# Kernel optimization log

Hardware: AMD Instinct MI355X
Metric: run time of the kernel (lower is better)

Reference implementation:

```python
import jax, jax.numpy as jnp
import numpy as np

NUM_SRC = 100000
NUM_DST = 50000
E = 1200000
IN_FEATS = 128
H = 4
D = 16


def setup_inputs() -> dict:
    key = jax.random.key(0)
    ks = jax.random.split(key, 8)
    feat = jax.random.normal(ks[0], (NUM_DST + NUM_SRC, IN_FEATS), dtype=jnp.float32)
    edge_src = jax.random.randint(ks[1], (E,), 0, NUM_SRC)
    edge_dst = jax.random.randint(ks[2], (E,), 0, NUM_DST)
    # parameters (xavier-normal-ish scale)
    W = jax.random.normal(ks[3], (H * D, IN_FEATS), dtype=jnp.float32) * (2.0 / np.sqrt(IN_FEATS + H * D))
    attn_l = jax.random.normal(ks[4], (H, D), dtype=jnp.float32) * (2.0 / np.sqrt(1 + D))
    attn_r = jax.random.normal(ks[5], (H, D), dtype=jnp.float32) * (2.0 / np.sqrt(1 + D))
    bias = jnp.zeros((H * D,), dtype=jnp.float32)
    return {"feat": feat, "W": W, "attn_l": attn_l, "attn_r": attn_r,
            "bias": bias, "edge_src": edge_src, "edge_dst": edge_dst, "num_dst": NUM_DST}


def reference(feat, W, attn_l, attn_r, bias, edge_src, edge_dst, num_dst):
    negative_slope = 0.2
    n_heads, d_out = attn_l.shape
    # fc: [N, in] @ [in, H*D] -> [N, H, D]
    proj = (feat @ W.T).reshape(feat.shape[0], n_heads, d_out)
    feat_dst = proj[:num_dst]      # [num_dst, H, D]
    feat_src = proj[num_dst:]      # [num_src, H, D]
    el = jnp.einsum('nhd,hd->nh', feat_src, attn_l)  # [num_src, H]
    er = jnp.einsum('nhd,hd->nh', feat_dst, attn_r)  # [num_dst, H]
    # per-edge attention logits (u_add_v + leaky_relu)
    e = jax.nn.leaky_relu(el[edge_src] + er[edge_dst], negative_slope)  # [E, H]
    # segment softmax over destination neighborhoods
    m = jax.ops.segment_max(e, edge_dst, num_segments=num_dst)  # [num_dst, H]
    m = jnp.where(jnp.isfinite(m), m, 0.0)
    e_exp = jnp.exp(e - m[edge_dst])
    denom = jax.ops.segment_sum(e_exp, edge_dst, num_segments=num_dst)  # [num_dst, H]
    a = e_exp / denom[edge_dst]  # [E, H]
    # u_mul_e + sum scatter-aggregate
    msg = feat_src[edge_src] * a[:, :, None]  # [E, H, D]
    rst = jax.ops.segment_sum(msg, edge_dst, num_segments=num_dst)  # [num_dst, H, D]
    rst = rst + bias.reshape(1, n_heads, d_out)
    return rst
```

## Files before the change

kernel.cpp:

```cpp
#include <hip/hip_runtime.h>
#include <hip/hip_bf16.h>


#define NEG_SLOPE 0.2f
#define BSHIFT 7
#define BMASK  127
#define MAXBUK 512
#define FSH    12
#define FCAP   4096
#define EB     2048

typedef __attribute__((ext_vector_type(8))) short bf16x8;
typedef __attribute__((ext_vector_type(4))) float f32x4;

__device__ __forceinline__ short f2bf(float f) {
    unsigned u = __float_as_uint(f);
    unsigned r = (u + 0x7fffu + ((u >> 16) & 1u)) >> 16;
    return (short)r;
}
__device__ __forceinline__ unsigned pk2(float a, float b) {
    return (unsigned)(unsigned short)f2bf(a) | ((unsigned)(unsigned short)f2bf(b) << 16);
}

__global__ __launch_bounds__(256) void k_init(const float* __restrict__ W,
                                              short* __restrict__ Wb, int nW,
                                              int* __restrict__ bukcnt) {
    for (int i = threadIdx.x; i < nW; i += 256) Wb[i] = f2bf(W[i]);
    for (int i = threadIdx.x; i < MAXBUK; i += 256) bukcnt[i] = 0;
}

__global__ __launch_bounds__(256) void k_proj_bin(
        const float* __restrict__ feat, const short* __restrict__ Wb,
        const float* __restrict__ attn_l, const float* __restrict__ attn_r,
        unsigned short* __restrict__ projb, float* __restrict__ el, float* __restrict__ er,
        int num_tot, int num_dst, int binB,
        const int* __restrict__ es, const int* __restrict__ ed,
        int* __restrict__ bukcnt, unsigned* __restrict__ pairs, int E, int nbuk) {
    __shared__ __align__(16) char smem_[17408];
    if ((int)blockIdx.x >= binB) {
        unsigned short* fs = (unsigned short*)smem_;
        float* fsf = (float*)smem_;
        const int tid = threadIdx.x;
        const int nblk = ((int)blockIdx.x - binB) * 64;

#pragma unroll
        for (int it = 0; it < 4; it++) {
            int flat = it * 2048 + tid * 8;
            int row = flat >> 7;
            int col = flat & 127;
            int grow = nblk + row;
            if (grow >= num_tot) grow = num_tot - 1;
            const float4* src = (const float4*)(feat + (size_t)grow * 128 + col);
            float4 x = src[0], y = src[1];
            bf16x8 t;
            t[0] = f2bf(x.x); t[1] = f2bf(x.y); t[2] = f2bf(x.z); t[3] = f2bf(x.w);
            t[4] = f2bf(y.x); t[5] = f2bf(y.y); t[6] = f2bf(y.z); t[7] = f2bf(y.w);
            int slot = col >> 3;
            *(bf16x8*)&fs[row * 128 + ((slot ^ (row & 15)) << 3)] = t;
        }
        __syncthreads();

        const int lane = tid & 63;
        const int wv = tid >> 6;
        const int lr = lane & 15;
        const int lg = lane >> 4;

        bf16x8 afrag[4];
#pragma unroll
        for (int c = 0; c < 4; c++)
            afrag[c] = *(const bf16x8*)&fs[(wv * 16 + lr) * 128 + (((c * 4 + lg) ^ lr) << 3)];
        __syncthreads();

        f32x4 acc[4];
#pragma unroll
        for (int hh = 0; hh < 4; hh++) acc[hh] = f32x4{0.f, 0.f, 0.f, 0.f};
#pragma unroll
        for (int hh = 0; hh < 4; hh++) {
            const short* bp = Wb + (hh * 16 + lr) * 128 + lg * 8;
#pragma unroll
            for (int c = 0; c < 4; c++) {
                bf16x8 b = *(const bf16x8*)(bp + c * 32);
                acc[hh] = __builtin_amdgcn_mfma_f32_16x16x32_bf16(afrag[c], b, acc[hh], 0, 0, 0);
            }
        }

#pragma unroll
        for (int hh = 0; hh < 4; hh++)
#pragma unroll
            for (int r = 0; r < 4; r++)
                fsf[(wv * 16 + lg * 4 + r) * 68 + hh * 16 + lr] = acc[hh][r];
        __syncthreads();

        int row = tid >> 2, seg = tid & 3;
        int n = nblk + row;
        if (n < num_tot) {
            const float4* rp = (const float4*)&fsf[row * 68 + seg * 16];
            float4 v0 = rp[0], v1 = rp[1], v2 = rp[2], v3 = rp[3];
            bool is_dst = n < num_dst;
            const float* attn = is_dst ? attn_r : attn_l;
            const float4* ap = (const float4*)&attn[seg * 16];
            float4 a0 = ap[0], a1 = ap[1], a2 = ap[2], a3 = ap[3];
            float e = v0.x * a0.x + v0.y * a0.y + v0.z * a0.z + v0.w * a0.w
                    + v1.x * a1.x + v1.y * a1.y + v1.z * a1.z + v1.w * a1.w
                    + v2.x * a2.x + v2.y * a2.y + v2.z * a2.z + v2.w * a2.w
                    + v3.x * a3.x + v3.y * a3.y + v3.z * a3.z + v3.w * a3.w;
            if (is_dst) {
                er[(size_t)n * 4 + seg] = e;
            } else {
                int sN = n - num_dst;
                el[(size_t)sN * 4 + seg] = e;
                uint4 q0, q1;
                q0.x = pk2(v0.x, v0.y); q0.y = pk2(v0.z, v0.w);
                q0.z = pk2(v1.x, v1.y); q0.w = pk2(v1.z, v1.w);
                q1.x = pk2(v2.x, v2.y); q1.y = pk2(v2.z, v2.w);
                q1.z = pk2(v3.x, v3.y); q1.w = pk2(v3.z, v3.w);
                uint4* dst = (uint4*)(projb + (size_t)sN * 64 + seg * 16);
                dst[0] = q0; dst[1] = q1;
            }
        }
    } else {
        int* h = (int*)smem_;
        int* cur = (int*)(smem_ + 2048);
        const int tid = threadIdx.x;
        for (int i = tid; i < MAXBUK; i += 256) h[i] = 0;
        __syncthreads();
        int base = (int)blockIdx.x * EB;
        int rd[EB / 256], rs[EB / 256];
#pragma unroll
        for (int i = 0; i < EB / 256; i++) {
            int idx = base + tid + i * 256;
            if (idx < E) {
                rd[i] = ed[idx];
                rs[i] = es[idx];
                atomicAdd(&h[rd[i] >> BSHIFT], 1);
            } else {
                rd[i] = -1;
            }
        }
        __syncthreads();
        for (int i = tid; i < nbuk; i += 256)
            cur[i] = h[i] ? ((i << FSH) + atomicAdd(&bukcnt[i], h[i])) : 0;
        __syncthreads();
#pragma unroll
        for (int i = 0; i < EB / 256; i++) {
            if (rd[i] >= 0) {
                int d = rd[i];
                int bk = d >> BSHIFT;
                int pos = atomicAdd(&cur[bk], 1);
                if (pos < ((bk + 1) << FSH))
                    pairs[pos] = (unsigned)rs[i] | ((unsigned)(d & BMASK) << 25);
            }
        }
    }
}

__global__ __launch_bounds__(256) void k_fillb(unsigned* __restrict__ pairs,
                                               const int* __restrict__ bukcnt,
                                               int* __restrict__ offs,
                                               int* __restrict__ counts, int nd) {
    __shared__ unsigned lp[FCAP];
    __shared__ int h[128], ex[128], cur[128];
    int b = blockIdx.x;
    int s = b << FSH;
    int cnt = bukcnt[b];
    if (cnt > FCAP) cnt = FCAP;
    if (threadIdx.x < 128) h[threadIdx.x] = 0;
    __syncthreads();
    for (int i = threadIdx.x; i < cnt; i += 256) {
        unsigned v = pairs[s + i];
        lp[i] = v;
        atomicAdd(&h[v >> 25], 1);
    }
    __syncthreads();
    if (threadIdx.x < 128) ex[threadIdx.x] = h[threadIdx.x];
    __syncthreads();
    for (int off = 1; off < 128; off <<= 1) {
        int v = (threadIdx.x >= off && threadIdx.x < 128) ? ex[threadIdx.x - off] : 0;
        __syncthreads();
        if (threadIdx.x < 128) ex[threadIdx.x] += v;
        __syncthreads();
    }
    if (threadIdx.x < 128) {
        int e = ex[threadIdx.x] - h[threadIdx.x];
        cur[threadIdx.x] = e;
        int d = (b << BSHIFT) + threadIdx.x;
        if (d < nd) { offs[d] = s + e; counts[d] = h[threadIdx.x]; }
    }
    __syncthreads();
    for (int i = threadIdx.x; i < cnt; i += 256) {
        unsigned v = lp[i];
        int r = atomicAdd(&cur[v >> 25], 1);
        pairs[s + r] = v & 0x1FFFFFFu;
    }
}

__global__ __launch_bounds__(256) void k_agg(
        const unsigned* __restrict__ csr_src, const int* __restrict__ offs,
        const int* __restrict__ counts, const float* __restrict__ el,
        const float* __restrict__ er, const unsigned short* __restrict__ projb,
        const float* __restrict__ bias, float* __restrict__ out, int nd) {
    int wave = (blockIdx.x * 256 + threadIdx.x) >> 6;
    int lane = threadIdx.x & 63;
    if (wave >= nd) return;
    int d = wave;
    int j = lane & 15, h = lane >> 4;
    int q = lane >> 4, cq = lane & 15;
    int hsrc = (cq >> 2) << 4;
    int start = offs[d], deg = counts[d];
    float er_h = er[d * 4 + h];

    float den = 0.f, a0 = 0.f, a1 = 0.f, a2 = 0.f, a3 = 0.f;
    for (int base = 0; base < deg; base += 16) {
        int cend = deg - base;
        if (cend > 16) cend = 16;
        int sidx = 0;
        float w = 0.f;
        if (j < cend) {
            sidx = (int)csr_src[start + base + j];
            float t = el[sidx * 4 + h] + er_h;
            t = t > 0.f ? t : NEG_SLOPE * t;
            w = __expf(fminf(t, 60.f));
        }
        den += w;
        if (cend == 16) {
#pragma unroll
            for (int t4 = 0; t4 < 4; t4++) {
                int e = 4 * t4 + q;
                int s2 = __shfl(sidx, e);
                float w2 = __shfl(w, hsrc | e);
                uint2 pv = *(const uint2*)(projb + (size_t)s2 * 64 + cq * 4);
                a0 += w2 * __uint_as_float(pv.x << 16);
                a1 += w2 * __uint_as_float(pv.x & 0xffff0000u);
                a2 += w2 * __uint_as_float(pv.y << 16);
                a3 += w2 * __uint_as_float(pv.y & 0xffff0000u);
            }
        } else {
            int steps = (cend + 3) >> 2;
            for (int t4 = 0; t4 < steps; t4++) {
                int e = 4 * t4 + q;
                int s2 = __shfl(sidx, e & 15);
                float w2 = __shfl(w, hsrc | (e & 15));
                uint2 pv = *(const uint2*)(projb + (size_t)s2 * 64 + cq * 4);
                a0 += w2 * __uint_as_float(pv.x << 16);
                a1 += w2 * __uint_as_float(pv.x & 0xffff0000u);
                a2 += w2 * __uint_as_float(pv.y << 16);
                a3 += w2 * __uint_as_float(pv.y & 0xffff0000u);
            }
        }
    }

    den += __shfl_xor(den, 1);
    den += __shfl_xor(den, 2);
    den += __shfl_xor(den, 4);
    den += __shfl_xor(den, 8);
    float den_h = __shfl(den, hsrc);

    a0 += __shfl_xor(a0, 16); a0 += __shfl_xor(a0, 32);
    a1 += __shfl_xor(a1, 16); a1 += __shfl_xor(a1, 32);
    a2 += __shfl_xor(a2, 16); a2 += __shfl_xor(a2, 32);
    a3 += __shfl_xor(a3, 16); a3 += __shfl_xor(a3, 32);

    if (q == 0) {
        float rden = den_h > 0.f ? 1.f / den_h : 0.f;
        float4 o;
        o.x = a0 * rden + bias[cq * 4];
        o.y = a1 * rden + bias[cq * 4 + 1];
        o.z = a2 * rden + bias[cq * 4 + 2];
        o.w = a3 * rden + bias[cq * 4 + 3];
        *(float4*)&out[(size_t)d * 64 + cq * 4] = o;
    }
}

extern "C" void kernel_launch(void* const* d_in, const int* in_sizes, int n_in,
                              void* d_out, int out_size, void* d_ws, size_t ws_size,
                              hipStream_t stream) {
    const float* feat   = (const float*)d_in[0];
    const float* W      = (const float*)d_in[1];
    const float* attn_l = (const float*)d_in[2];
    const float* attn_r = (const float*)d_in[3];
    const float* bias   = (const float*)d_in[4];
    const int*   es     = (const int*)d_in[5];
    const int*   ed     = (const int*)d_in[6];

    const int HD      = in_sizes[2];
    const int in_f    = in_sizes[1] / HD;
    const int num_dst = out_size / HD;
    const int num_tot = in_sizes[0] / in_f;
    const int num_src = num_tot - num_dst;
    const int E       = in_sizes[5];

    float* out = (float*)d_out;

    const int NBUK = (num_dst + BMASK) >> BSHIFT;

    unsigned short* projb = (unsigned short*)d_ws;
    float*    el       = (float*)(projb + (size_t)num_src * 64);
    float*    er       = el + (size_t)num_src * 4;
    int*      counts   = (int*)(er + (size_t)num_dst * 4);
    int*      offs     = counts + num_dst;
    int*      bukcnt   = offs + num_dst;
    unsigned* pairs    = (unsigned*)(bukcnt + MAXBUK);
    short*    Wb       = (short*)(pairs + ((size_t)NBUK << FSH));

    const int projB = (num_tot + 63) / 64;
    const int binB  = (E + EB - 1) / EB;

    k_init<<<1, 256, 0, stream>>>(W, Wb, HD * in_f, bukcnt);

    k_proj_bin<<<binB + projB, 256, 0, stream>>>(
        feat, Wb, attn_l, attn_r, projb, el, er, num_tot, num_dst, binB,
        es, ed, bukcnt, pairs, E, NBUK);

    k_fillb<<<NBUK, 256, 0, stream>>>(pairs, bukcnt, offs, counts, num_dst);

    k_agg<<<(num_dst * 64 + 255) / 256, 256, 0, stream>>>(
        pairs, offs, counts, el, er, projb, bias, out, num_dst);
}
```

Measured before the change: 104.4 us.

## Software-pipeline projection tiles per block and vectorize edge index loads

Each projection block now handles four 64-row tiles and prefetches the next tile's features into registers while the MFMA and epilogue of the current tile run, using separate shared buffers for input and output staging. The aim is to hide global load latency and cut block count. The binning path now reads eight contiguous edges per thread with int4 loads instead of strided scalar loads. This raises LDS use and register pressure, which may lower occupancy, and the edge-to-thread assignment changes the order in which pairs are written.

```diff
diff --git a/kernel.cpp b/kernel.cpp
--- a/kernel.cpp
+++ b/kernel.cpp
@@ -9,6 +9,7 @@
 #define FSH    12
 #define FCAP   4096
 #define EB     2048
+#define TILES  4
 
 typedef __attribute__((ext_vector_type(8))) short bf16x8;
 typedef __attribute__((ext_vector_type(4))) float f32x4;
@@ -36,87 +37,115 @@
         int num_tot, int num_dst, int binB,
         const int* __restrict__ es, const int* __restrict__ ed,
         int* __restrict__ bukcnt, unsigned* __restrict__ pairs, int E, int nbuk) {
-    __shared__ __align__(16) char smem_[17408];
+    __shared__ __align__(16) char smem_[33792];
     if ((int)blockIdx.x >= binB) {
         unsigned short* fs = (unsigned short*)smem_;
-        float* fsf = (float*)smem_;
+        float* fsf = (float*)(smem_ + 16384);
         const int tid = threadIdx.x;
-        const int nblk = ((int)blockIdx.x - binB) * 64;
-
-#pragma unroll
-        for (int it = 0; it < 4; it++) {
-            int flat = it * 2048 + tid * 8;
-            int row = flat >> 7;
-            int col = flat & 127;
-            int grow = nblk + row;
-            if (grow >= num_tot) grow = num_tot - 1;
-            const float4* src = (const float4*)(feat + (size_t)grow * 128 + col);
-            float4 x = src[0], y = src[1];
-            bf16x8 t;
-            t[0] = f2bf(x.x); t[1] = f2bf(x.y); t[2] = f2bf(x.z); t[3] = f2bf(x.w);
-            t[4] = f2bf(y.x); t[5] = f2bf(y.y); t[6] = f2bf(y.z); t[7] = f2bf(y.w);
-            int slot = col >> 3;
-            *(bf16x8*)&fs[row * 128 + ((slot ^ (row & 15)) << 3)] = t;
-        }
-        __syncthreads();
+        const int pb = (int)blockIdx.x - binB;
 
         const int lane = tid & 63;
         const int wv = tid >> 6;
         const int lr = lane & 15;
         const int lg = lane >> 4;
 
-        bf16x8 afrag[4];
-#pragma unroll
-        for (int c = 0; c < 4; c++)
-            afrag[c] = *(const bf16x8*)&fs[(wv * 16 + lr) * 128 + (((c * 4 + lg) ^ lr) << 3)];
-        __syncthreads();
-
-        f32x4 acc[4];
-#pragma unroll
-        for (int hh = 0; hh < 4; hh++) acc[hh] = f32x4{0.f, 0.f, 0.f, 0.f};
-#pragma unroll
-        for (int hh = 0; hh < 4; hh++) {
-            const short* bp = Wb + (hh * 16 + lr) * 128 + lg * 8;
-#pragma unroll
-            for (int c = 0; c < 4; c++) {
-                bf16x8 b = *(const bf16x8*)(bp + c * 32);
-                acc[hh] = __builtin_amdgcn_mfma_f32_16x16x32_bf16(afrag[c], b, acc[hh], 0, 0, 0);
-            }
-        }
-
-#pragma unroll
-        for (int hh = 0; hh < 4; hh++)
-#pragma unroll
-            for (int r = 0; r < 4; r++)
-                fsf[(wv * 16 + lg * 4 + r) * 68 + hh * 16 + lr] = acc[hh][r];
-        __syncthreads();
-
-        int row = tid >> 2, seg = tid & 3;
-        int n = nblk + row;
-        if (n < num_tot) {
-            const float4* rp = (const float4*)&fsf[row * 68 + seg * 16];
-            float4 v0 = rp[0], v1 = rp[1], v2 = rp[2], v3 = rp[3];
-            bool is_dst = n < num_dst;
-            const float* attn = is_dst ? attn_r : attn_l;
-            const float4* ap = (const float4*)&attn[seg * 16];
-            float4 a0 = ap[0], a1 = ap[1], a2 = ap[2], a3 = ap[3];
-            float e = v0.x * a0.x + v0.y * a0.y + v0.z * a0.z + v0.w * a0.w
-                    + v1.x * a1.x + v1.y * a1.y + v1.z * a1.z + v1.w * a1.w
-                    + v2.x * a2.x + v2.y * a2.y + v2.z * a2.z + v2.w * a2.w
-                    + v3.x * a3.x + v3.y * a3.y + v3.z * a3.z + v3.w * a3.w;
-            if (is_dst) {
-                er[(size_t)n * 4 + seg] = e;
-            } else {
-                int sN = n - num_dst;
-                el[(size_t)sN * 4 + seg] = e;
-                uint4 q0, q1;
-                q0.x = pk2(v0.x, v0.y); q0.y = pk2(v0.z, v0.w);
-                q0.z = pk2(v1.x, v1.y); q0.w = pk2(v1.z, v1.w);
-                q1.x = pk2(v2.x, v2.y); q1.y = pk2(v2.z, v2.w);
-                q1.z = pk2(v3.x, v3.y); q1.w = pk2(v3.z, v3.w);
-                uint4* dst = (uint4*)(projb + (size_t)sN * 64 + seg * 16);
-                dst[0] = q0; dst[1] = q1;
-            }
+        float4 pf[8];
+        int st_row[4], st_col[4];
+#pragma unroll
+        for (int it = 0; it < 4; it++) {
+            int flat = it * 2048 + tid * 8;
+            st_row[it] = flat >> 7;
+            st_col[it] = flat & 127;
+        }
+
+        auto issue = [&](int t) {
+            int nb = pb * (TILES * 64) + t * 64;
+#pragma unroll
+            for (int it = 0; it < 4; it++) {
+                int grow = nb + st_row[it];
+                if (grow >= num_tot) grow = num_tot - 1;
+                const float4* src = (const float4*)(feat + (size_t)grow * 128 + st_col[it]);
+                pf[it * 2] = src[0];
+                pf[it * 2 + 1] = src[1];
+            }
+        };
+        auto commit = [&]() {
+#pragma unroll
+            for (int it = 0; it < 4; it++) {
+                float4 x = pf[it * 2], y = pf[it * 2 + 1];
+                bf16x8 t;
+                t[0] = f2bf(x.x); t[1] = f2bf(x.y); t[2] = f2bf(x.z); t[3] = f2bf(x.w);
+                t[4] = f2bf(y.x); t[5] = f2bf(y.y); t[6] = f2bf(y.z); t[7] = f2bf(y.w);
+                int slot = st_col[it] >> 3;
+                int row = st_row[it];
+                *(bf16x8*)&fs[row * 128 + ((slot ^ (row & 15)) << 3)] = t;
+            }
+        };
+
+        issue(0);
+        commit();
+
+        for (int t = 0; t < TILES; t++) {
+            __syncthreads();
+
+            bf16x8 afrag[4];
+#pragma unroll
+            for (int c = 0; c < 4; c++)
+                afrag[c] = *(const bf16x8*)&fs[(wv * 16 + lr) * 128 + (((c * 4 + lg) ^ lr) << 3)];
+
+            if (t + 1 < TILES) issue(t + 1);
+
+            f32x4 acc[4];
+#pragma unroll
+            for (int hh = 0; hh < 4; hh++) acc[hh] = f32x4{0.f, 0.f, 0.f, 0.f};
+#pragma unroll
+            for (int hh = 0; hh < 4; hh++) {
+                const short* bp = Wb + (hh * 16 + lr) * 128 + lg * 8;
+#pragma unroll
+                for (int c = 0; c < 4; c++) {
+                    bf16x8 b = *(const bf16x8*)(bp + c * 32);
+                    acc[hh] = __builtin_amdgcn_mfma_f32_16x16x32_bf16(afrag[c], b, acc[hh], 0, 0, 0);
+                }
+            }
+
+#pragma unroll
+            for (int hh = 0; hh < 4; hh++)
+#pragma unroll
+                for (int r = 0; r < 4; r++)
+                    fsf[(wv * 16 + lg * 4 + r) * 68 + hh * 16 + lr] = acc[hh][r];
+            __syncthreads();
+
+            {
+                int row = tid >> 2, seg = tid & 3;
+                int n = pb * (TILES * 64) + t * 64 + row;
+                if (n < num_tot) {
+                    const float4* rp = (const float4*)&fsf[row * 68 + seg * 16];
+                    float4 v0 = rp[0], v1 = rp[1], v2 = rp[2], v3 = rp[3];
+                    bool is_dst = n < num_dst;
+                    const float* attn = is_dst ? attn_r : attn_l;
+                    const float4* ap = (const float4*)&attn[seg * 16];
+                    float4 a0 = ap[0], a1 = ap[1], a2 = ap[2], a3 = ap[3];
+                    float e = v0.x * a0.x + v0.y * a0.y + v0.z * a0.z + v0.w * a0.w
+                            + v1.x * a1.x + v1.y * a1.y + v1.z * a1.z + v1.w * a1.w
+                            + v2.x * a2.x + v2.y * a2.y + v2.z * a2.z + v2.w * a2.w
+                            + v3.x * a3.x + v3.y * a3.y + v3.z * a3.z + v3.w * a3.w;
+                    if (is_dst) {
+                        er[(size_t)n * 4 + seg] = e;
+                    } else {
+                        int sN = n - num_dst;
+                        el[(size_t)sN * 4 + seg] = e;
+                        uint4 q0, q1;
+                        q0.x = pk2(v0.x, v0.y); q0.y = pk2(v0.z, v0.w);
+                        q0.z = pk2(v1.x, v1.y); q0.w = pk2(v1.z, v1.w);
+                        q1.x = pk2(v2.x, v2.y); q1.y = pk2(v2.z, v2.w);
+                        q1.z = pk2(v3.x, v3.y); q1.w = pk2(v3.z, v3.w);
+                        uint4* dst = (uint4*)(projb + (size_t)sN * 64 + seg * 16);
+                        dst[0] = q0; dst[1] = q1;
+                    }
+                }
+            }
+
+            if (t + 1 < TILES) commit();
         }
     } else {
         int* h = (int*)smem_;
@@ -125,16 +154,29 @@
         for (int i = tid; i < MAXBUK; i += 256) h[i] = 0;
         __syncthreads();
         int base = (int)blockIdx.x * EB;
-        int rd[EB / 256], rs[EB / 256];
-#pragma unroll
-        for (int i = 0; i < EB / 256; i++) {
-            int idx = base + tid + i * 256;
-            if (idx < E) {
-                rd[i] = ed[idx];
-                rs[i] = es[idx];
-                atomicAdd(&h[rd[i] >> BSHIFT], 1);
-            } else {
-                rd[i] = -1;
+        int rd[8], rs[8];
+        if (base + EB <= E) {
+            const int4* edp = (const int4*)(ed + base + tid * 8);
+            const int4* esp = (const int4*)(es + base + tid * 8);
+            int4 d0 = edp[0], d1 = edp[1];
+            int4 s0 = esp[0], s1 = esp[1];
+            rd[0] = d0.x; rd[1] = d0.y; rd[2] = d0.z; rd[3] = d0.w;
+            rd[4] = d1.x; rd[5] = d1.y; rd[6] = d1.z; rd[7] = d1.w;
+            rs[0] = s0.x; rs[1] = s0.y; rs[2] = s0.z; rs[3] = s0.w;
+            rs[4] = s1.x; rs[5] = s1.y; rs[6] = s1.z; rs[7] = s1.w;
+#pragma unroll
+            for (int i = 0; i < 8; i++) atomicAdd(&h[rd[i] >> BSHIFT], 1);
+        } else {
+#pragma unroll
+            for (int i = 0; i < 8; i++) {
+                int idx = base + tid * 8 + i;
+                if (idx < E) {
+                    rd[i] = ed[idx];
+                    rs[i] = es[idx];
+                    atomicAdd(&h[rd[i] >> BSHIFT], 1);
+                } else {
+                    rd[i] = -1;
+                }
             }
         }
         __syncthreads();
@@ -142,7 +184,7 @@
             cur[i] = h[i] ? ((i << FSH) + atomicAdd(&bukcnt[i], h[i])) : 0;
         __syncthreads();
 #pragma unroll
-        for (int i = 0; i < EB / 256; i++) {
+        for (int i = 0; i < 8; i++) {
             if (rd[i] >= 0) {
                 int d = rd[i];
                 int bk = d >> BSHIFT;
@@ -302,7 +344,7 @@
     unsigned* pairs    = (unsigned*)(bukcnt + MAXBUK);
     short*    Wb       = (short*)(pairs + ((size_t)NBUK << FSH));
 
-    const int projB = (num_tot + 63) / 64;
+    const int projB = (num_tot + TILES * 64 - 1) / (TILES * 64);
     const int binB  = (E + EB - 1) / EB;
 
     k_init<<<1, 256, 0, stream>>>(W, Wb, HD * in_f, bukcnt);
```

Result: faster. 102.3 us (median of 2 runs) (-2.0%).

## Stage binned edge pairs in shared memory for coalesced bucket writes

Applied to the files above, without the earlier changes.

The binning blocks now load edge indices with vectorized int4 reads, prefix-scan the per-block bucket histogram in LDS, and place each pair into a locally sorted LDS buffer along with its global address. A final pass writes pairs out in local order so that consecutive threads write to contiguous runs within a bucket, replacing scattered global stores. This costs more shared memory per block (which may lower occupancy for the projection blocks sharing the allocation) and adds a log-step scan with many barriers.

```diff
diff --git a/kernel.cpp b/kernel.cpp
--- a/kernel.cpp
+++ b/kernel.cpp
@@ -36,7 +36,7 @@
         int num_tot, int num_dst, int binB,
         const int* __restrict__ es, const int* __restrict__ ed,
         int* __restrict__ bukcnt, unsigned* __restrict__ pairs, int E, int nbuk) {
-    __shared__ __align__(16) char smem_[17408];
+    __shared__ __align__(16) char smem_[24576];
     if ((int)blockIdx.x >= binB) {
         unsigned short* fs = (unsigned short*)smem_;
         float* fsf = (float*)smem_;
@@ -119,36 +119,78 @@
             }
         }
     } else {
-        int* h = (int*)smem_;
-        int* cur = (int*)(smem_ + 2048);
+        unsigned* lp = (unsigned*)smem_;
+        int* addr  = (int*)(smem_ + 8192);
+        int* h     = (int*)(smem_ + 16384);
+        int* sh    = (int*)(smem_ + 18432);
+        int* cur   = (int*)(smem_ + 20480);
+        int* gbase = (int*)(smem_ + 22528);
         const int tid = threadIdx.x;
         for (int i = tid; i < MAXBUK; i += 256) h[i] = 0;
         __syncthreads();
         int base = (int)blockIdx.x * EB;
-        int rd[EB / 256], rs[EB / 256];
-#pragma unroll
-        for (int i = 0; i < EB / 256; i++) {
-            int idx = base + tid + i * 256;
-            if (idx < E) {
-                rd[i] = ed[idx];
-                rs[i] = es[idx];
-                atomicAdd(&h[rd[i] >> BSHIFT], 1);
-            } else {
-                rd[i] = -1;
-            }
-        }
-        __syncthreads();
-        for (int i = tid; i < nbuk; i += 256)
-            cur[i] = h[i] ? ((i << FSH) + atomicAdd(&bukcnt[i], h[i])) : 0;
-        __syncthreads();
-#pragma unroll
-        for (int i = 0; i < EB / 256; i++) {
+        int cnt_blk = E - base; if (cnt_blk > EB) cnt_blk = EB;
+        int rd[8], rs[8];
+        if (base + EB <= E) {
+            const int4* edp = (const int4*)(ed + base + tid * 8);
+            const int4* esp = (const int4*)(es + base + tid * 8);
+            int4 d0 = edp[0], d1 = edp[1];
+            int4 s0 = esp[0], s1 = esp[1];
+            rd[0] = d0.x; rd[1] = d0.y; rd[2] = d0.z; rd[3] = d0.w;
+            rd[4] = d1.x; rd[5] = d1.y; rd[6] = d1.z; rd[7] = d1.w;
+            rs[0] = s0.x; rs[1] = s0.y; rs[2] = s0.z; rs[3] = s0.w;
+            rs[4] = s1.x; rs[5] = s1.y; rs[6] = s1.z; rs[7] = s1.w;
+#pragma unroll
+            for (int i = 0; i < 8; i++) atomicAdd(&h[rd[i] >> BSHIFT], 1);
+        } else {
+#pragma unroll
+            for (int i = 0; i < 8; i++) {
+                int idx = base + tid * 8 + i;
+                if (idx < E) {
+                    rd[i] = ed[idx];
+                    rs[i] = es[idx];
+                    atomicAdd(&h[rd[i] >> BSHIFT], 1);
+                } else {
+                    rd[i] = -1;
+                }
+            }
+        }
+        __syncthreads();
+        {
+            int i0 = tid, i1 = tid + 256;
+            sh[i0] = h[i0]; sh[i1] = h[i1];
+            __syncthreads();
+            for (int off = 1; off < MAXBUK; off <<= 1) {
+                int v0 = (i0 >= off) ? sh[i0 - off] : 0;
+                int v1 = (i1 >= off) ? sh[i1 - off] : 0;
+                __syncthreads();
+                sh[i0] += v0; sh[i1] += v1;
+                __syncthreads();
+            }
+            int c0 = h[i0], c1 = h[i1];
+            cur[i0] = sh[i0] - c0;  cur[i1] = sh[i1] - c1;
+            if (c0 > 0 && i0 < nbuk) gbase[i0] = (i0 << FSH) + atomicAdd(&bukcnt[i0], c0);
+            if (c1 > 0 && i1 < nbuk) gbase[i1] = (i1 << FSH) + atomicAdd(&bukcnt[i1], c1);
+        }
+        __syncthreads();
+#pragma unroll
+        for (int i = 0; i < 8; i++) {
             if (rd[i] >= 0) {
                 int d = rd[i];
                 int bk = d >> BSHIFT;
-                int pos = atomicAdd(&cur[bk], 1);
-                if (pos < ((bk + 1) << FSH))
-                    pairs[pos] = (unsigned)rs[i] | ((unsigned)(d & BMASK) << 25);
+                int r = atomicAdd(&cur[bk], 1);
+                lp[r] = (unsigned)rs[i] | ((unsigned)(d & BMASK) << 25);
+                int a = gbase[bk] + (r - (sh[bk] - h[bk]));
+                addr[r] = (a < ((bk + 1) << FSH)) ? a : -1;
+            }
+        }
+        __syncthreads();
+#pragma unroll
+        for (int k = 0; k < 8; k++) {
+            int i = tid + k * 256;
+            if (i < cnt_blk) {
+                int a = addr[i];
+                if (a >= 0) pairs[a] = lp[i];
             }
         }
     }
```

New measurement: 104.7 us. About the same (+0.3%).
